# Performance work log

Measured on AMD Instinct MI355X. Metric: run time of the kernel, lower is better.

## Reference

```python
import jax, jax.numpy as jnp
import numpy as np

N_NODES = 100000
N_RADIAL = 16  # columns 0..15
N_CONICAL = 16  # columns 16..31


def setup_inputs() -> dict:
    key = jax.random.key(0)
    k1, k2, k3, k4 = jax.random.split(key, 4)
    x = jax.random.normal(k1, (N_NODES, 32), dtype=jnp.float32)
    edge_index = jax.random.randint(k2, (2, 1600000), 0, N_NODES, dtype=jnp.int32)
    W1 = jax.random.normal(k3, (32, 128), dtype=jnp.float32) * 0.1
    b1 = jnp.zeros((128,), dtype=jnp.float32)
    W2 = jax.random.normal(k4, (128, 32), dtype=jnp.float32) * 0.1
    b2 = jnp.zeros((32,), dtype=jnp.float32)
    return {"x": x, "edge_index": edge_index, "W1": W1, "b1": b1, "W2": W2, "b2": b2}


def reference(x, edge_index, W1, b1, W2, b2):
    # slice radial / conical feature channels
    radial = x[:, :N_RADIAL]            # [N, 16]
    conical = x[:, N_RADIAL:N_RADIAL + N_CONICAL]  # [N, 16]

    i, j = edge_index[0], edge_index[1]
    rows = jnp.concatenate([i, j])      # symmetrized COO rows [2E]
    cols = jnp.concatenate([j, i])      # symmetrized COO cols [2E]

    # coalesce()+sparse.mm == segment-sum over all (duplicated) entries
    neighbor_sum = jax.ops.segment_sum(conical[cols], rows, num_segments=N_NODES)  # [N, 16]
    deg = jax.ops.segment_sum(jnp.ones_like(rows, dtype=x.dtype), rows, num_segments=N_NODES)
    deg = jnp.clip(deg, 1.0)[:, None]   # bincount(...).clamp(min=1)
    agg = neighbor_sum / deg            # mean aggregation

    combined = jnp.concatenate([radial, agg], axis=1)  # [N, 32]
    h = jax.nn.relu(combined @ W1 + b1)
    out = h @ W2 + b2                   # [N, 32]
    return out
```

## Files before the change

### kernel.cpp

```cpp
#include <hip/hip_runtime.h>
#include <hip/hip_bf16.h>
#include <hip/hip_fp16.h>

#define N_NODES  100000
#define N_RADIAL 16
#define N_CONICAL 16

#define NPB    256
#define NBKT   ((N_NODES + NPB - 1) / NPB)
#define NBLK_A 256
#define BTHR   512
#define SUBCAP 96
#define BKTSTRIDE (NBLK_A * SUBCAP)
#define CAP    10240

__global__ __launch_bounds__(BTHR) void binfuse_kernel(
    const int* __restrict__ idx, const float* __restrict__ x,
    __half2* __restrict__ xcon2,
    const float* __restrict__ W1, const float* __restrict__ W2,
    float* __restrict__ W1t, float* __restrict__ W2t,
    unsigned int* __restrict__ binned, int* __restrict__ cnts,
    int chunk, int total, int E) {
    int b = blockIdx.x, tid = threadIdx.x;
    if (b >= NBLK_A) {
        int pb = b - NBLK_A;
        if (pb == 0) {
            for (int i = tid; i < 4096; i += BTHR) {
                int c = i >> 7, k = i & 127;
                W1t[k * 32 + c] = W1[i];
                int kk = i >> 5, o = i & 31;
                W2t[o * 128 + kk] = W2[i];
            }
        } else {
            int t = (pb - 1) * BTHR + tid;
            if (t < N_NODES * 8) {
                int n = t >> 3, p = t & 7;
                const float2* xp = (const float2*)x;
                float2 v = xp[n * 16 + 8 + p];
                xcon2[t] = __floats2half2_rn(v.x, v.y);
            }
        }
        return;
    }

    __shared__ int cur[NBKT];
    for (int i = tid; i < NBKT; i += BTHR)
        cur[i] = i * BKTSTRIDE + b * SUBCAP;
    __syncthreads();

    int lo = b * chunk;
    int hi = min(lo + chunk, total);
    for (int d = lo + tid; d < hi; d += BTHR) {
        int row = idx[d];
        int col = (d < E) ? idx[d + E] : idx[d - E];
        int bkt = row >> 8;
        int p = atomicAdd(&cur[bkt], 1);
        binned[p] = ((unsigned int)(row & 255) << 17) | (unsigned int)col;
    }
    __syncthreads();

    for (int i = tid; i < NBKT; i += BTHR)
        cnts[i * NBLK_A + b] = cur[i] - (i * BKTSTRIDE + b * SUBCAP);
}

__global__ __launch_bounds__(1024, 2) void agg_kernel(
    const __half* __restrict__ xcon, const int* __restrict__ cnts,
    const unsigned int* __restrict__ binned, __half* __restrict__ agg) {
    __shared__ unsigned int sedge[CAP];
    __shared__ int scnt[NPB];
    __shared__ int soff[NPB];
    int b = blockIdx.x, tid = threadIdx.x;
    if (tid < NPB) scnt[tid] = 0;
    __syncthreads();

    int sub = tid >> 2, l = tid & 2 * 2 - 1;
    int sc  = cnts[b * NBLK_A + sub];
    unsigned int base = (unsigned int)b * BKTSTRIDE + (unsigned int)sub * SUBCAP;

    for (int j = l; j < sc; j += 4)
        atomicAdd(&scnt[binned[base + j] >> 17], 1);
    __syncthreads();

    if (tid < NPB) soff[tid] = scnt[tid];
    __syncthreads();
    for (int off = 1; off < NPB; off <<= 1) {
        int y = 0;
        if (tid < NPB && tid >= off) y = soff[tid - off];
        __syncthreads();
        if (tid < NPB) soff[tid] += y;
        __syncthreads();
    }
    if (tid < NPB) soff[tid] -= scnt[tid];
    __syncthreads();

    for (int j = l; j < sc; j += 4) {
        unsigned int p = binned[base + j];
        int pos = atomicAdd(&soff[p >> 17], 1);
        sedge[pos] = p & 0x1FFFFu;
    }
    __syncthreads();

    if (tid < 2 * NPB) {
        int nl = tid >> 1, q = tid & 1;
        int c  = scnt[nl];
        int s0 = soff[nl] - c;
        float a0 = 0.f, a1 = 0.f, a2 = 0.f, a3 = 0.f;
        float a4 = 0.f, a5 = 0.f, a6 = 0.f, a7 = 0.f;
        #pragma unroll 2
        for (int k = 0; k < c; k++) {
            int col = (int)sedge[s0 + k];
            uint4 raw = ((const uint4*)(xcon + (size_t)col * 16))[q];
            float2 f0 = __half22float2(*(const __half2*)&raw.x);
            float2 f1 = __half22float2(*(const __half2*)&raw.y);
            float2 f2 = __half22float2(*(const __half2*)&raw.z);
            float2 f3 = __half22float2(*(const __half2*)&raw.w);
            a0 += f0.x; a1 += f0.y; a2 += f1.x; a3 += f1.y;
            a4 += f2.x; a5 += f2.y; a6 += f3.x; a7 += f3.y;
        }
        int n = b * NPB + nl;
        if (n < N_NODES) {
            float inv = 1.0f / (float)max(c, 1);
            __half2 h0 = __floats2half2_rn(a0 * inv, a1 * inv);
            __half2 h1 = __floats2half2_rn(a2 * inv, a3 * inv);
            __half2 h2 = __floats2half2_rn(a4 * inv, a5 * inv);
            __half2 h3 = __floats2half2_rn(a6 * inv, a7 * inv);
            uint4 st;
            st.x = *(unsigned int*)&h0; st.y = *(unsigned int*)&h1;
            st.z = *(unsigned int*)&h2; st.w = *(unsigned int*)&h3;
            *(uint4*)(agg + (size_t)n * 16 + q * 8) = st;
        }
    }
}

__global__ __launch_bounds__(512, 4) void mlp_kernel(
    const float* __restrict__ x, const __half* __restrict__ agg,
    const float* __restrict__ W1t, const float* __restrict__ b1,
    const float* __restrict__ W2t, const float* __restrict__ b2,
    float* __restrict__ out, int N) {
    __shared__ __half2 H2[64 * 64];
    int tid  = threadIdx.x;
    int lane = tid & 63;
    int ws   = __builtin_amdgcn_readfirstlane(tid >> 6);
    int n    = blockIdx.x * 64 + lane;
    int nc   = min(n, N - 1);

    float comb[32];
    const float4* xr = (const float4*)(x + (size_t)nc * 32);
    #pragma unroll
    for (int c = 0; c < 4; c++) {
        float4 v = xr[c];
        comb[c*4+0] = v.x; comb[c*4+1] = v.y;
        comb[c*4+2] = v.z; comb[c*4+3] = v.w;
    }
    const __half2* ar = (const __half2*)(agg + (size_t)nc * 16);
    #pragma unroll
    for (int c = 0; c < 8; c++) {
        float2 f = __half22float2(ar[c]);
        comb[16 + 2*c]     = f.x;
        comb[16 + 2*c + 1] = f.y;
    }

    #pragma unroll
    for (int i = 0; i < 16; i += 2) {
        int k0 = ws * 16 + i;
        const float* w1a = W1t + k0 * 32;
        const float* w1b = w1a + 32;
        float ha = b1[k0], hb = b1[k0 + 1];
        #pragma unroll
        for (int c = 0; c < 32; c++) {
            ha = fmaf(comb[c], w1a[c], ha);
            hb = fmaf(comb[c], w1b[c], hb);
        }
        ha = fmaxf(ha, 0.f); hb = fmaxf(hb, 0.f);
        H2[(k0 >> 1) * 64 + lane] = __floats2half2_rn(ha, hb);
    }
    __syncthreads();

    int o0 = ws * 4;
    const float* w20 = W2t + (o0 + 0) * 128;
    const float* w21 = W2t + (o0 + 1) * 128;
    const float* w22 = W2t + (o0 + 2) * 128;
    const float* w23 = W2t + (o0 + 3) * 128;
    float acc0 = b2[o0+0], acc1 = b2[o0+1], acc2 = b2[o0+2], acc3 = b2[o0+3];
    #pragma unroll 8
    for (int kp = 0; kp < 64; kp++) {
        float2 h = __half22float2(H2[kp * 64 + lane]);
        int k0 = 2 * kp;
        acc0 = fmaf(h.x, w20[k0], acc0); acc0 = fmaf(h.y, w20[k0+1], acc0);
        acc1 = fmaf(h.x, w21[k0], acc1); acc1 = fmaf(h.y, w21[k0+1], acc1);
        acc2 = fmaf(h.x, w22[k0], acc2); acc2 = fmaf(h.y, w22[k0+1], acc2);
        acc3 = fmaf(h.x, w23[k0], acc3); acc3 = fmaf(h.y, w23[k0+1], acc3);
    }
    if (n < N) {
        float* op = out + (size_t)n * 32 + o0;
        op[0] = acc0; op[1] = acc1; op[2] = acc2; op[3] = acc3;
    }
}

extern "C" void kernel_launch(void* const* d_in, const int* in_sizes, int n_in,
                              void* d_out, int out_size, void* d_ws, size_t ws_size,
                              hipStream_t stream) {
    const float* x   = (const float*)d_in[0];
    const int*   idx = (const int*)d_in[1];
    const float* W1  = (const float*)d_in[2];
    const float* b1  = (const float*)d_in[3];
    const float* W2  = (const float*)d_in[4];
    const float* b2  = (const float*)d_in[5];
    float* out = (float*)d_out;

    const int E = in_sizes[1] / 2;
    const int total = 2 * E;
    const int chunk = (total + NBLK_A - 1) / NBLK_A;

    char* base = (char*)d_ws;
    __half*       agg    = (__half*)base;
    __half*       xcon   = (__half*)(base + 3203072);
    float*        W1t    = (float*)(base + 6406144);
    float*        W2t    = (float*)(base + 6422528);
    int*          cnts   = (int*)(base + 6438912);
    unsigned int* binned = (unsigned int*)(base + 6839296);

    int pack_blocks = (N_NODES * 8 + BTHR - 1) / BTHR;
    binfuse_kernel<<<NBLK_A + 1 + pack_blocks, BTHR, 0, stream>>>(
        idx, x, (__half2*)xcon, W1, W2, W1t, W2t,
        binned, cnts, chunk, total, E);
    agg_kernel<<<NBKT, 1024, 0, stream>>>(xcon, cnts, binned, agg);
    mlp_kernel<<<(N_NODES + 63) / 64, 512, 0, stream>>>(
        x, agg, W1t, b1, W2t, b2, out, N_NODES);
}
```

Before: 158.4 us.

## Vectorize edge binning with int4 loads and fixed chunks; widen xcon packing

The binning phase now runs 500 blocks, each with a fixed 6400-edge chunk, and reads rows and cols as int4 vectors. The col offset is hoisted per block, which is only valid because no chunk straddles the E boundary. Per-block sub-bucket capacity drops to 64, and the aggregation kernel reads two entries per sub-bucket instead of four to match. The fp16 packing of the conical features moves from float2 to float4 loads. Together these cut scalar load instructions and branching. The cost is hardcoding the chunk size, which assumes exactly 3.2M edges, and a smaller per-bucket capacity that could overflow on skewed inputs.

Result: slower. 175.4 us (+10.7%).

```diff
diff --git a/kernel.cpp b/kernel.cpp
--- a/kernel.cpp
+++ b/kernel.cpp
@@ -8,9 +8,10 @@
 
 #define NPB    256
 #define NBKT   ((N_NODES + NPB - 1) / NPB)
-#define NBLK_A 256
+#define NBLK_A 500
 #define BTHR   512
-#define SUBCAP 96
+#define CHUNK  6400
+#define SUBCAP 64
 #define BKTSTRIDE (NBLK_A * SUBCAP)
 #define CAP    10240
 
@@ -33,11 +34,14 @@
             }
         } else {
             int t = (pb - 1) * BTHR + tid;
-            if (t < N_NODES * 8) {
-                int n = t >> 3, p = t & 7;
-                const float2* xp = (const float2*)x;
-                float2 v = xp[n * 16 + 8 + p];
-                xcon2[t] = __floats2half2_rn(v.x, v.y);
+            if (t < N_NODES * 4) {
+                int n = t >> 2, p = t & 3;
+                float4 v = *((const float4*)(x + (size_t)n * 32 + 16) + p);
+                __half2 h0 = __floats2half2_rn(v.x, v.y);
+                __half2 h1 = __floats2half2_rn(v.z, v.w);
+                uint2 st;
+                st.x = *(unsigned int*)&h0; st.y = *(unsigned int*)&h1;
+                *(uint2*)(xcon2 + 2 * t) = st;
             }
         }
         return;
@@ -48,14 +52,20 @@
         cur[i] = i * BKTSTRIDE + b * SUBCAP;
     __syncthreads();
 
-    int lo = b * chunk;
-    int hi = min(lo + chunk, total);
-    for (int d = lo + tid; d < hi; d += BTHR) {
-        int row = idx[d];
-        int col = (d < E) ? idx[d + E] : idx[d - E];
-        int bkt = row >> 8;
-        int p = atomicAdd(&cur[bkt], 1);
-        binned[p] = ((unsigned int)(row & 255) << 17) | (unsigned int)col;
+    int lo = b * CHUNK;
+    int cofs = (lo >= E) ? -E : E;
+    #pragma unroll 1
+    for (int d0 = lo + (tid << 2); d0 < lo + CHUNK; d0 += BTHR * 4) {
+        int4 r = *(const int4*)(idx + d0);
+        int4 c = *(const int4*)(idx + d0 + cofs);
+        int p0 = atomicAdd(&cur[r.x >> 8], 1);
+        int p1 = atomicAdd(&cur[r.y >> 8], 1);
+        int p2 = atomicAdd(&cur[r.z >> 8], 1);
+        int p3 = atomicAdd(&cur[r.w >> 8], 1);
+        binned[p0] = ((unsigned int)(r.x & 255) << 17) | (unsigned int)c.x;
+        binned[p1] = ((unsigned int)(r.y & 255) << 17) | (unsigned int)c.y;
+        binned[p2] = ((unsigned int)(r.z & 255) << 17) | (unsigned int)c.z;
+        binned[p3] = ((unsigned int)(r.w & 255) << 17) | (unsigned int)c.w;
     }
     __syncthreads();
 
@@ -73,11 +83,11 @@
     if (tid < NPB) scnt[tid] = 0;
     __syncthreads();
 
-    int sub = tid >> 2, l = tid & 2 * 2 - 1;
-    int sc  = cnts[b * NBLK_A + sub];
+    int sub = tid >> 1, l = tid & 1;
+    int sc  = (sub < NBLK_A) ? cnts[b * NBLK_A + sub] : 0;
     unsigned int base = (unsigned int)b * BKTSTRIDE + (unsigned int)sub * SUBCAP;
 
-    for (int j = l; j < sc; j += 4)
+    for (int j = l; j < sc; j += 2)
         atomicAdd(&scnt[binned[base + j] >> 17], 1);
     __syncthreads();
 
@@ -93,7 +103,7 @@
     if (tid < NPB) soff[tid] -= scnt[tid];
     __syncthreads();
 
-    for (int j = l; j < sc; j += 4) {
+    for (int j = l; j < sc; j += 2) {
         unsigned int p = binned[base + j];
         int pos = atomicAdd(&soff[p >> 17], 1);
         sedge[pos] = p & 0x1FFFFu;
@@ -210,7 +220,6 @@
 
     const int E = in_sizes[1] / 2;
     const int total = 2 * E;
-    const int chunk = (total + NBLK_A - 1) / NBLK_A;
 
     char* base = (char*)d_ws;
     __half*       agg    = (__half*)base;
@@ -218,12 +227,12 @@
     float*        W1t    = (float*)(base + 6406144);
     float*        W2t    = (float*)(base + 6422528);
     int*          cnts   = (int*)(base + 6438912);
-    unsigned int* binned = (unsigned int*)(base + 6839296);
-
-    int pack_blocks = (N_NODES * 8 + BTHR - 1) / BTHR;
+    unsigned int* binned = (unsigned int*)(base + 7225344);
+
+    int pack_blocks = (N_NODES * 4 + BTHR - 1) / BTHR;
     binfuse_kernel<<<NBLK_A + 1 + pack_blocks, BTHR, 0, stream>>>(
         idx, x, (__half2*)xcon, W1, W2, W1t, W2t,
-        binned, cnts, chunk, total, E);
+        binned, cnts, CHUNK, total, E);
     agg_kernel<<<NBKT, 1024, 0, stream>>>(xcon, cnts, binned, agg);
     mlp_kernel<<<(N_NODES + 63) / 64, 512, 0, stream>>>(
         x, agg, W1t, b1, W2t, b2, out, N_NODES);
```
